# Optimization experiments

Measured on AMD Instinct MI355X. Metric: run time of the kernel, lower is better.

Reference implementation:

```python
import jax, jax.numpy as jnp
import numpy as np

HEADS = 16
CHUNK = 128  # chunked (mathematically exact) form of the causal cumsum linear attention
EPS = 0.001


def _linear_attention(q, k, v):
    # q, k, v: (B, H, L, d); q, k already SiLU-featurized
    B, H, L, d = q.shape
    Nc = L // CHUNK
    qc = q.reshape(B, H, Nc, CHUNK, d)
    kc = k.reshape(B, H, Nc, CHUNK, d)
    vc = v.reshape(B, H, Nc, CHUNK, d)

    # inter-chunk running state: S = cumsum of k (x) v over previous chunks, z = cumsum of k
    kv_chunk = jnp.einsum('bhncd,bhnce->bhnde', kc, vc)        # (B,H,Nc,d,d)
    S = jnp.cumsum(kv_chunk, axis=2) - kv_chunk                 # exclusive cumsum
    k_sum = kc.sum(axis=3)                                      # (B,H,Nc,d)
    z = jnp.cumsum(k_sum, axis=2) - k_sum                       # exclusive cumsum

    # intra-chunk causal part
    scores = jnp.einsum('bhnid,bhnjd->bhnij', qc, kc)           # (B,H,Nc,C,C)
    mask = jnp.tril(jnp.ones((CHUNK, CHUNK), dtype=bool))
    scores = jnp.where(mask, scores, jnp.zeros((), scores.dtype))
    num = jnp.einsum('bhnij,bhnje->bhnie', scores, vc)
    num = num + jnp.einsum('bhnid,bhnde->bhnie', qc, S)

    k_cum_local = jnp.cumsum(kc, axis=3)                        # within-chunk cumsum of k
    den = jnp.einsum('bhnid,bhnid->bhni', qc, k_cum_local)
    den = den + jnp.einsum('bhnid,bhnd->bhni', qc, z)

    out = num / jnp.maximum(den, EPS)[..., None]
    return out.reshape(B, H, L, d)


def setup_inputs() -> dict:
    key = jax.random.key(0)
    ks = jax.random.split(key, 9)
    D = 1024
    B, L = 4, 2048
    s = 0.02  # init scale
    return {
        'x':  jax.random.normal(ks[0], (B, L, D), dtype=jnp.float32),
        'Wq': jax.random.normal(ks[1], (D, D), dtype=jnp.float32) * s,
        'bq': jnp.zeros((D,), dtype=jnp.float32),
        'Wk': jax.random.normal(ks[2], (D, D), dtype=jnp.float32) * s,
        'bk': jnp.zeros((D,), dtype=jnp.float32),
        'Wv': jax.random.normal(ks[3], (D, D), dtype=jnp.float32) * s,
        'bv': jnp.zeros((D,), dtype=jnp.float32),
        'Wo': jax.random.normal(ks[4], (D, D), dtype=jnp.float32) * s,
        'bo': jnp.zeros((D,), dtype=jnp.float32),
    }


def reference(x, Wq, bq, Wk, bk, Wv, bv, Wo, bo):
    B, L, D = x.shape
    H = HEADS
    d = D // H
    # torch Linear: y = x @ W.T + b
    q = jax.nn.silu(x @ Wq.T + bq).reshape(B, L, H, d).transpose(0, 2, 1, 3)
    k = jax.nn.silu(x @ Wk.T + bk).reshape(B, L, H, d).transpose(0, 2, 1, 3)
    v = (x @ Wv.T + bv).reshape(B, L, H, d).transpose(0, 2, 1, 3)
    out = _linear_attention(q, k, v)                  # (B,H,L,d)
    out = out.transpose(0, 2, 1, 3).reshape(B, L, D)
    return out @ Wo.T + bo
```

## Files before the change

kernel.cpp:

```cpp
#include <hip/hip_runtime.h>
#include <math.h>

#define D_MODEL 1024
#define HEADS   16
#define HDIM    64
#define CHUNK   128
#define B_SZ    4
#define L_SEQ   2048
#define NCHUNK  16
#define NTOK    8192
#define EPS_DEN 1e-3f

typedef _Float16 half8 __attribute__((ext_vector_type(8)));
typedef float    f32x4 __attribute__((ext_vector_type(4)));

__device__ __forceinline__ void gld_lds16(const void* g, void* l) {
    __builtin_amdgcn_global_load_lds(
        (const __attribute__((address_space(1))) void*)g,
        (__attribute__((address_space(3))) void*)l, 16, 0, 0);
}

__global__ __launch_bounds__(256) void prep(
    const float* __restrict__ x,  const float* __restrict__ Wq,
    const float* __restrict__ Wk, const float* __restrict__ Wv,
    const float* __restrict__ Wo, const float* __restrict__ bq,
    const float* __restrict__ bk,
    _Float16* __restrict__ x2,  _Float16* __restrict__ w2q,
    _Float16* __restrict__ w2k, _Float16* __restrict__ wv16,
    _Float16* __restrict__ wo16, float* __restrict__ bqk) {
    const int bid = blockIdx.x;
    if (bid < 5120) {
        const float* src; _Float16* dst; int t;
        if (bid < 4096)      { src = x;  dst = x2;  t = bid * 256 + threadIdx.x; }
        else if (bid < 4608) { src = Wq; dst = w2q; t = (bid - 4096) * 256 + threadIdx.x; }
        else                 { src = Wk; dst = w2k; t = (bid - 4608) * 256 + threadIdx.x; }
        int m = t >> 7, kc = (t & 127) << 3;
        const float* s = src + (size_t)m * 1024 + kc;
        f32x4 a = *(const f32x4*)s;
        f32x4 b = *(const f32x4*)(s + 4);
        float xs[8] = {a.x, a.y, a.z, a.w, b.x, b.y, b.z, b.w};
        half8 hi, lo;
        #pragma unroll
        for (int u = 0; u < 8; ++u) {
            _Float16 h = (_Float16)xs[u];
            hi[u] = h;
            lo[u] = (_Float16)(xs[u] - (float)h);
        }
        *(half8*)(dst + (size_t)m * 2048 + kc)        = hi;
        *(half8*)(dst + (size_t)m * 2048 + 1024 + kc) = lo;
    } else if (bid < 6144) {
        const float* src; _Float16* dst; int t;
        if (bid < 5632) { src = Wv; dst = wv16; t = (bid - 5120) * 256 + threadIdx.x; }
        else            { src = Wo; dst = wo16; t = (bid - 5632) * 256 + threadIdx.x; }
        int m = t >> 7, kc = (t & 127) << 3;
        const float* s = src + (size_t)m * 1024 + kc;
        f32x4 a = *(const f32x4*)s;
        f32x4 b = *(const f32x4*)(s + 4);
        float xs[8] = {a.x, a.y, a.z, a.w, b.x, b.y, b.z, b.w};
        half8 hv;
        #pragma unroll
        for (int u = 0; u < 8; ++u) hv[u] = (_Float16)xs[u];
        *(half8*)(dst + (size_t)m * 1024 + kc) = hv;
    } else {
        int i = (bid - 6144) * 256 + threadIdx.x;
        bqk[i] = (i < 1024) ? bq[i] : bk[i - 1024];
    }
}

__global__ __launch_bounds__(256, 4) void gemm_qkv(
    const _Float16* __restrict__ A,
    const _Float16* __restrict__ Bqk,
    const _Float16* __restrict__ Bv,
    const float* __restrict__ bqk, const float* __restrict__ bv,
    float* __restrict__ Q32, float* __restrict__ K32,
    _Float16* __restrict__ Q16, _Float16* __restrict__ K16,
    _Float16* __restrict__ V16, float* __restrict__ ksum) {
    __shared__ __align__(16) _Float16 sA[4096];
    __shared__ __align__(16) _Float16 sB[4096];
    __shared__ __align__(16) _Float16 sC16[32 * 136];
    __shared__ float sksum[2][128];

    const int cb   = blockIdx.y;
    const int isqk = (cb < 16);
    const int isk  = (cb >= 8 && cb < 16);
    const int tid  = threadIdx.x;
    const int lane = tid & 63;
    const int w    = tid >> 6;
    const int row0 = blockIdx.x * 128;
    const int col0 = cb * 128;
    const int wm   = (w & 1) * 64;
    const int wn   = (w >> 1) * 64;

    const _Float16* B = isqk ? Bqk : Bv;
    const int ldb     = isqk ? 2048 : 1024;
    const int bcol0   = isqk ? col0 : col0 - 2048;
    const int kits    = isqk ? 96 : 32;

    const int ch0 = w * 64 + lane;
    const int rS0 = ch0 >> 2;
    const int cS0 = (ch0 & 3) ^ ((rS0 >> 1) & 3);
    const int ch1 = ch0 + 256;
    const int rS1 = ch1 >> 2;
    const int cS1 = (ch1 & 3) ^ ((rS1 >> 1) & 3);

    f32x4 acc[4][4];
    #pragma unroll
    for (int i = 0; i < 4; ++i)
        #pragma unroll
        for (int j = 0; j < 4; ++j) { f32x4 z = {0.f, 0.f, 0.f, 0.f}; acc[i][j] = z; }

    const int ml = lane & 15;
    const int kg = lane >> 4;
    int offA[4], offB[4];
    #pragma unroll
    for (int i = 0; i < 4; ++i) {
        int r  = wm + i * 16 + ml;
        offA[i] = r * 32 + (kg ^ ((r >> 1) & 3)) * 8;
        int rn = wn + i * 16 + ml;
        offB[i] = rn * 32 + (kg ^ ((rn >> 1) & 3)) * 8;
    }

    for (int kit = 0; kit < kits; ++kit) {
        const int k0   = kit * 32;
        const int acol = (k0 < 2048) ? k0 : k0 - 2048;
        const int bcol = (k0 < 1024) ? k0 : k0 - 1024;

        gld_lds16(A + (size_t)(row0 + rS0) * 2048 + acol + cS0 * 8, &sA[w * 512]);
        gld_lds16(A + (size_t)(row0 + rS1) * 2048 + acol + cS1 * 8, &sA[2048 + w * 512]);
        gld_lds16(B + (size_t)(bcol0 + rS0) * ldb + bcol + cS0 * 8, &sB[w * 512]);
        gld_lds16(B + (size_t)(bcol0 + rS1) * ldb + bcol + cS1 * 8, &sB[2048 + w * 512]);
        __syncthreads();

        half8 af[4], bf[4];
        #pragma unroll
        for (int i = 0; i < 4; ++i) {
            af[i] = *(const half8*)&sA[offA[i]];
            bf[i] = *(const half8*)&sB[offB[i]];
        }
        #pragma unroll
        for (int i = 0; i < 4; ++i)
            #pragma unroll
            for (int j = 0; j < 4; ++j)
                acc[i][j] = __builtin_amdgcn_mfma_f32_16x16x32_f16(af[i], bf[j], acc[i][j], 0, 0, 0);
        __syncthreads();
    }

    const int colq = isqk ? ((col0 < 1024) ? col0 : col0 - 1024) : (col0 - 2048);
    float*    Y32  = (col0 < 1024) ? Q32 : K32;
    _Float16* Y16  = isqk ? ((col0 < 1024) ? Q16 : K16) : V16;

    const int rg = lane >> 4;
    #pragma unroll
    for (int j = 0; j < 4; ++j) {
        const float bvb = isqk ? bqk[col0 + wn + j * 16 + ml]
                               : bv[colq + wn + j * 16 + ml];
        const int nn = colq + wn + j * 16 + ml;
        #pragma unroll
        for (int i = 0; i < 4; ++i) {
            #pragma unroll
            for (int t = 0; t < 4; ++t) {
                float vv = acc[i][j][t] + bvb;
                if (isqk) {
                    vv = vv / (1.f + expf(-vv));
                    int mm = row0 + wm + i * 16 + rg * 4 + t;
                    Y32[(size_t)mm * 1024 + nn] = vv;
                }
                acc[i][j][t] = vv;
            }
        }
    }

    if (isk) {
        #pragma unroll
        for (int j = 0; j < 4; ++j) {
            float ps = 0.f;
            #pragma unroll
            for (int i = 0; i < 4; ++i)
                #pragma unroll
                for (int t = 0; t < 4; ++t) ps += acc[i][j][t];
            ps += __shfl_xor(ps, 16, 64);
            ps += __shfl_xor(ps, 32, 64);
            if (kg == 0) sksum[wm >> 6][wn + j * 16 + ml] = ps;
        }
        __syncthreads();
        if (tid < 128) {
            const int b = row0 >> 11;
            const int n = (row0 >> 7) & 15;
            const int cg = colq + tid;
            const int h = cg >> 6, f = cg & 63;
            ksum[(size_t)(((b * 16 + h) * 16 + n)) * 64 + f] =
                sksum[0][tid] + sksum[1][tid];
        }
        __syncthreads();
    }

    for (int s = 0; s < 4; ++s) {
        if ((wm == 0) == (s < 2)) {
            const int ib = (s & 1) * 2;
            #pragma unroll
            for (int ii = 0; ii < 2; ++ii)
                #pragma unroll
                for (int j = 0; j < 4; ++j)
                    #pragma unroll
                    for (int t = 0; t < 4; ++t) {
                        int lr = ii * 16 + rg * 4 + t;
                        sC16[lr * 136 + wn + j * 16 + ml] = (_Float16)acc[ib + ii][j][t];
                    }
        }
        __syncthreads();
        #pragma unroll
        for (int u = 0; u < 2; ++u) {
            int c = u * 256 + tid;
            int r = c >> 4, cc = (c & 15) * 8;
            half8 hv = *(const half8*)&sC16[r * 136 + cc];
            *(half8*)(Y16 + (size_t)(row0 + 32 * s + r) * 1024 + colq + cc) = hv;
        }
        __syncthreads();
    }
}

__global__ __launch_bounds__(256, 4) void gemm_out(
    const _Float16* __restrict__ A,
    const _Float16* __restrict__ B,
    const float* __restrict__ bias,
    float* __restrict__ Y) {
    __shared__ __align__(16) _Float16 sA[4096];
    __shared__ __align__(16) _Float16 sB[2048];

    const int tid  = threadIdx.x;
    const int lane = tid & 63;
    const int w    = tid >> 6;
    const int row0 = blockIdx.x * 128;
    const int col0 = blockIdx.y * 64;

    const int ch0 = w * 64 + lane;
    const int rS0 = ch0 >> 2;
    const int cS0 = (ch0 & 3) ^ ((rS0 >> 1) & 3);
    const int ch1 = ch0 + 256;
    const int rS1 = ch1 >> 2;
    const int cS1 = (ch1 & 3) ^ ((rS1 >> 1) & 3);

    f32x4 acc[2][4];
    #pragma unroll
    for (int i = 0; i < 2; ++i)
        #pragma unroll
        for (int j = 0; j < 4; ++j) { f32x4 z = {0.f, 0.f, 0.f, 0.f}; acc[i][j] = z; }

    const int ml = lane & 15;
    const int kg = lane >> 4;
    int offA[2], offB[4];
    #pragma unroll
    for (int i = 0; i < 2; ++i) {
        int r  = w * 32 + i * 16 + ml;
        offA[i] = r * 32 + (kg ^ ((r >> 1) & 3)) * 8;
    }
    #pragma unroll
    for (int j = 0; j < 4; ++j) {
        int rn = j * 16 + ml;
        offB[j] = rn * 32 + (kg ^ ((rn >> 1) & 3)) * 8;
    }

    for (int kit = 0; kit < 32; ++kit) {
        const int k0 = kit * 32;
        gld_lds16(A + (size_t)(row0 + rS0) * 1024 + k0 + cS0 * 8, &sA[w * 512]);
        gld_lds16(A + (size_t)(row0 + rS1) * 1024 + k0 + cS1 * 8, &sA[2048 + w * 512]);
        gld_lds16(B + (size_t)(col0 + rS0) * 1024 + k0 + cS0 * 8, &sB[w * 512]);
        __syncthreads();

        half8 af[2], bf[4];
        #pragma unroll
        for (int i = 0; i < 2; ++i) af[i] = *(const half8*)&sA[offA[i]];
        #pragma unroll
        for (int j = 0; j < 4; ++j) bf[j] = *(const half8*)&sB[offB[j]];
        #pragma unroll
        for (int i = 0; i < 2; ++i)
            #pragma unroll
            for (int j = 0; j < 4; ++j)
                acc[i][j] = __builtin_amdgcn_mfma_f32_16x16x32_f16(af[i], bf[j], acc[i][j], 0, 0, 0);
        __syncthreads();
    }

    const int rg = lane >> 4;
    #pragma unroll
    for (int j = 0; j < 4; ++j) {
        const int nn = col0 + j * 16 + ml;
        const float bvb = bias[nn];
        #pragma unroll
        for (int i = 0; i < 2; ++i) {
            #pragma unroll
            for (int t = 0; t < 4; ++t) {
                int mm = row0 + w * 32 + i * 16 + rg * 4 + t;
                Y[(size_t)mm * 1024 + nn] = acc[i][j][t] * 64.f + bvb;
            }
        }
    }
}

__global__ __launch_bounds__(256) void chunk_stats(
    const _Float16* __restrict__ k16g, const _Float16* __restrict__ v16g,
    float* __restrict__ kvT) {
    const int blk = blockIdx.x;
    const int n = blk & 15, bh = blk >> 4, h = bh & 15, b = bh >> 4;
    const size_t base = ((size_t)b * L_SEQ + (size_t)n * CHUNK) * D_MODEL + (size_t)h * HDIM;

    __shared__ __align__(16) _Float16 sv[64 * 136];
    __shared__ __align__(16) _Float16 sk[64 * 136];

    const int tid = threadIdx.x;
    #pragma unroll
    for (int p = 0; p < 4; ++p) {
        int idx = p * 256 + tid;
        int j = idx >> 3, c = idx & 7;
        half8 vv = *(const half8*)(v16g + base + (size_t)j * D_MODEL + c * 8);
        half8 kk = *(const half8*)(k16g + base + (size_t)j * D_MODEL + c * 8);
        #pragma unroll
        for (int u = 0; u < 8; ++u) {
            sv[(c * 8 + u) * 136 + j] = vv[u];
            sk[(c * 8 + u) * 136 + j] = kk[u];
        }
    }
    __syncthreads();

    const int lane = tid & 63;
    const int w    = tid >> 6;
    const int ml   = lane & 15;
    const int kg   = lane >> 4;

    f32x4 acc[4];
    #pragma unroll
    for (int ft = 0; ft < 4; ++ft) { f32x4 z = {0.f,0.f,0.f,0.f}; acc[ft] = z; }
    #pragma unroll
    for (int ft = 0; ft < 4; ++ft)
        #pragma unroll
        for (int kit = 0; kit < 4; ++kit) {
            half8 af = *(const half8*)&sv[(w * 16 + ml) * 136 + kit * 32 + kg * 8];
            half8 bf = *(const half8*)&sk[(ft * 16 + ml) * 136 + kit * 32 + kg * 8];
            acc[ft] = __builtin_amdgcn_mfma_f32_16x16x32_f16(af, bf, acc[ft], 0, 0, 0);
        }
    float* o = kvT + (size_t)blk * 4096;
    #pragma unroll
    for (int ft = 0; ft < 4; ++ft)
        #pragma unroll
        for (int t = 0; t < 4; ++t) {
            int e = w * 16 + kg * 4 + t;
            o[e * 64 + ft * 16 + ml] = acc[ft][t];
        }
}

__global__ __launch_bounds__(256) void scan_chunks(float* __restrict__ kvT,
                                                   float* __restrict__ ksum) {
    const int bh  = blockIdx.x >> 4;
    const int seg = blockIdx.x & 15;
    const int idx = seg * 256 + threadIdx.x;
    float* base = kvT + (size_t)bh * NCHUNK * 4096 + idx;
    float run = 0.f;
    #pragma unroll
    for (int nn = 0; nn < NCHUNK; ++nn) {
        float t = base[(size_t)nn * 4096];
        base[(size_t)nn * 4096] = run;
        run += t;
    }
    if (seg == 0 && threadIdx.x < 64) {
        float* zb = ksum + (size_t)bh * NCHUNK * 64 + threadIdx.x;
        float r2 = 0.f;
        #pragma unroll
        for (int nn = 0; nn < NCHUNK; ++nn) {
            float t = zb[nn * 64];
            zb[nn * 64] = r2;
            r2 += t;
        }
    }
}

__global__ __launch_bounds__(256) void den_kernel(
    const float* __restrict__ qf32, const float* __restrict__ kf32,
    const float* __restrict__ zg, float* __restrict__ deng) {
    const int blk = blockIdx.x;
    const int n = blk & 15, bh = blk >> 4, h = bh & 15, b = bh >> 4;
    const size_t base = ((size_t)b * L_SEQ + (size_t)n * CHUNK) * D_MODEL + (size_t)h * HDIM;

    __shared__ float skk[128 * 64];
    __shared__ float part[4 * 64];

    const int tid = threadIdx.x;
    #pragma unroll
    for (int p = 0; p < 8; ++p) {
        int idx = p * 256 + tid;
        int j = idx >> 4, fc = (idx & 15) * 4;
        *(f32x4*)&skk[j * 64 + fc] = *(const f32x4*)(kf32 + base + (size_t)j * D_MODEL + fc);
    }
    __syncthreads();

    const int w = tid >> 6, lane = tid & 63;
    float ps = 0.f;
    for (int j = w * 32; j < w * 32 + 32; ++j) ps += skk[j * 64 + lane];
    part[w * 64 + lane] = ps;
    __syncthreads();

    float acc = zg[(size_t)blk * 64 + lane];
    for (int w2 = 0; w2 < w; ++w2) acc += part[w2 * 64 + lane];

    float* dout = deng + ((size_t)(b * 16 + h)) * L_SEQ + n * CHUNK;
    for (int jj = 0; jj < 32; ++jj) {
        int j = w * 32 + jj;
        acc += skk[j * 64 + lane];
        float d = qf32[base + (size_t)j * D_MODEL + lane] * acc;
        #pragma unroll
        for (int off = 32; off > 0; off >>= 1) d += __shfl_xor(d, off, 64);
        if (lane == 0) dout[j] = d;
    }
}

__global__ __launch_bounds__(256) void attn_core(
    const _Float16* __restrict__ q16g, const _Float16* __restrict__ k16g,
    const _Float16* __restrict__ v16g, const float* __restrict__ STg,
    const float* __restrict__ deng, _Float16* __restrict__ O16) {
    const int blk = blockIdx.x;
    const int n = blk & 15, bh = blk >> 4, h = bh & 15, b = bh >> 4;
    const size_t base = ((size_t)b * L_SEQ + (size_t)n * CHUNK) * D_MODEL + (size_t)h * HDIM;

    __shared__ __align__(16) _Float16 sq [128 * 72];
    __shared__ __align__(16) _Float16 sk [128 * 72];
    __shared__ __align__(16) _Float16 sv [64 * 136];
    __shared__ __align__(16) _Float16 sS [64 * 72];
    __shared__ __align__(16) _Float16 ssc[64 * 136];
    __shared__ float sden[128];

    const int tid = threadIdx.x;
    #pragma unroll
    for (int p = 0; p < 4; ++p) {
        int idx = p * 256 + tid;
        int j = idx >> 3, c = idx & 7;
        *(half8*)&sq[j * 72 + c * 8] = *(const half8*)(q16g + base + (size_t)j * D_MODEL + c * 8);
        *(half8*)&sk[j * 72 + c * 8] = *(const half8*)(k16g + base + (size_t)j * D_MODEL + c * 8);
        half8 vv = *(const half8*)(v16g + base + (size_t)j * D_MODEL + c * 8);
        #pragma unroll
        for (int u = 0; u < 8; ++u) sv[(c * 8 + u) * 136 + j] = vv[u];
    }
    #pragma unroll
    for (int p = 0; p < 2; ++p) {
        int idx = p * 256 + tid;
        int e = idx >> 3, c = idx & 7;
        f32x4 a = *(const f32x4*)(STg + (size_t)blk * 4096 + e * 64 + c * 8);
        f32x4 b4 = *(const f32x4*)(STg + (size_t)blk * 4096 + e * 64 + c * 8 + 4);
        half8 hv;
        hv[0] = (_Float16)a.x;  hv[1] = (_Float16)a.y;
        hv[2] = (_Float16)a.z;  hv[3] = (_Float16)a.w;
        hv[4] = (_Float16)b4.x; hv[5] = (_Float16)b4.y;
        hv[6] = (_Float16)b4.z; hv[7] = (_Float16)b4.w;
        *(half8*)&sS[e * 72 + c * 8] = hv;
    }
    if (tid < 128) sden[tid] = deng[((size_t)(b * 16 + h)) * L_SEQ + n * CHUNK + tid];
    __syncthreads();

    const int lane = tid & 63;
    const int w    = tid >> 6;
    const int ml   = lane & 15;
    const int kg   = lane >> 4;

    for (int h2 = 0; h2 < 2; ++h2) {
        const int r0 = h2 * 64 + w * 16;
        const int rowmax = r0 + 15;

        f32x4 acc1[8];
        #pragma unroll
        for (int nt = 0; nt < 8; ++nt) { f32x4 z = {0.f,0.f,0.f,0.f}; acc1[nt] = z; }
        #pragma unroll
        for (int nt = 0; nt < 8; ++nt) {
            if (nt * 16 <= rowmax) {
                #pragma unroll
                for (int kit = 0; kit < 2; ++kit) {
                    half8 af = *(const half8*)&sq[(r0 + ml) * 72 + kit * 32 + kg * 8];
                    half8 bf = *(const half8*)&sk[(nt * 16 + ml) * 72 + kit * 32 + kg * 8];
                    acc1[nt] = __builtin_amdgcn_mfma_f32_16x16x32_f16(af, bf, acc1[nt], 0, 0, 0);
                }
            }
        }
        #pragma unroll
        for (int nt = 0; nt < 8; ++nt) {
            #pragma unroll
            for (int t = 0; t < 4; ++t) {
                int lr = w * 16 + kg * 4 + t;
                int ig = h2 * 64 + lr;
                int jg = nt * 16 + ml;
                float val = (jg <= ig) ? acc1[nt][t] : 0.f;
                ssc[lr * 136 + jg] = (_Float16)val;
            }
        }
        __syncthreads();

        f32x4 acc2[4];
        #pragma unroll
        for (int et = 0; et < 4; ++et) { f32x4 z = {0.f,0.f,0.f,0.f}; acc2[et] = z; }
        const int nkit = (h2 == 0) ? 2 : 4;
        #pragma unroll
        for (int et = 0; et < 4; ++et) {
            for (int kit = 0; kit < nkit; ++kit) {
                half8 af = *(const half8*)&ssc[(w * 16 + ml) * 136 + kit * 32 + kg * 8];
                half8 bf = *(const half8*)&sv[(et * 16 + ml) * 136 + kit * 32 + kg * 8];
                acc2[et] = __builtin_amdgcn_mfma_f32_16x16x32_f16(af, bf, acc2[et], 0, 0, 0);
            }
            #pragma unroll
            for (int kit = 0; kit < 2; ++kit) {
                half8 af = *(const half8*)&sq[(r0 + ml) * 72 + kit * 32 + kg * 8];
                half8 bf = *(const half8*)&sS[(et * 16 + ml) * 72 + kit * 32 + kg * 8];
                acc2[et] = __builtin_amdgcn_mfma_f32_16x16x32_f16(af, bf, acc2[et], 0, 0, 0);
            }
        }
        #pragma unroll
        for (int t = 0; t < 4; ++t) {
            int lr = w * 16 + kg * 4 + t;
            int ig = h2 * 64 + lr;
            float rc = 0.015625f / fmaxf(sden[ig], EPS_DEN);
            #pragma unroll
            for (int et = 0; et < 4; ++et) {
                int e = et * 16 + ml;
                O16[base + (size_t)ig * D_MODEL + e] = (_Float16)(acc2[et][t] * rc);
            }
        }
        __syncthreads();
    }
}

extern "C" void kernel_launch(void* const* d_in, const int* in_sizes, int n_in,
                              void* d_out, int out_size, void* d_ws, size_t ws_size,
                              hipStream_t stream) {
    const float* x  = (const float*)d_in[0];
    const float* Wq = (const float*)d_in[1];
    const float* bq = (const float*)d_in[2];
    const float* Wk = (const float*)d_in[3];
    const float* bk = (const float*)d_in[4];
    const float* Wv = (const float*)d_in[5];
    const float* bv = (const float*)d_in[6];
    const float* Wo = (const float*)d_in[7];
    const float* bo = (const float*)d_in[8];
    float* out = (float*)d_out;

    char* p = (char*)d_ws;
    _Float16* x2   = (_Float16*)p;  p += (size_t)NTOK * 2048 * 2;
    _Float16* w2q  = (_Float16*)p;  p += (size_t)1024 * 2048 * 2;
    _Float16* w2k  = (_Float16*)p;  p += (size_t)1024 * 2048 * 2;
    _Float16* wv16 = (_Float16*)p;  p += (size_t)1024 * 1024 * 2;
    _Float16* wo16 = (_Float16*)p;  p += (size_t)1024 * 1024 * 2;
    float* qf   = (float*)p;        p += (size_t)NTOK * 1024 * 4;
    float* kf   = (float*)p;        p += (size_t)NTOK * 1024 * 4;
    _Float16* q16 = (_Float16*)p;   p += (size_t)NTOK * 1024 * 2;
    _Float16* k16 = (_Float16*)p;   p += (size_t)NTOK * 1024 * 2;
    _Float16* v16 = (_Float16*)p;   p += (size_t)NTOK * 1024 * 2;
    float* kvT  = (float*)p;        p += (size_t)1024 * 4096 * 4;
    float* ksb  = (float*)p;        p += (size_t)1024 * 64 * 4;
    float* den  = (float*)p;        p += (size_t)B_SZ * HEADS * L_SEQ * 4;
    float* bqk  = (float*)p;        p += 2048 * 4;
    _Float16* attn16 = x2;

    prep<<<6152, 256, 0, stream>>>(x, Wq, Wk, Wv, Wo, bq, bk,
                                   x2, w2q, w2k, wv16, wo16, bqk);

    gemm_qkv<<<dim3(64, 24), 256, 0, stream>>>(x2, w2q, wv16, bqk, bv,
                                               qf, kf, q16, k16, v16, ksb);

    chunk_stats<<<1024, 256, 0, stream>>>(k16, v16, kvT);
    scan_chunks<<<1024, 256, 0, stream>>>(kvT, ksb);
    den_kernel<<<1024, 256, 0, stream>>>(qf, kf, ksb, den);
    attn_core<<<1024, 256, 0, stream>>>(q16, k16, v16, kvT, den, attn16);

    gemm_out<<<dim3(64, 16), 256, 0, stream>>>(attn16, wo16, bo, out);
}
```

Before: 348.1 us.

## Rework QKV GEMM into 256x256 tiles with 4-stage async LDS pipeline

Changes the QKV projection GEMM from 128x128 tiles with 256 threads to 256x256 tiles with 512 threads. A 4-buffer global_load_lds pipeline keeps three stages in flight, paced by vmcnt waits and a single barrier per k-step. A 1D swizzled block index groups blocks for L2 reuse. The k-sum reduction now writes directly without an LDS round trip. The aim is to cut per-iteration barrier stalls and raise operand reuse, at the cost of 128 KB of LDS and more accumulator registers per thread, which limits occupancy.

```diff
diff --git a/kernel.cpp b/kernel.cpp
--- a/kernel.cpp
+++ b/kernel.cpp
@@ -67,7 +67,7 @@
     }
 }
 
-__global__ __launch_bounds__(256, 4) void gemm_qkv(
+__global__ __launch_bounds__(512, 2) void gemm_qkv(
     const _Float16* __restrict__ A,
     const _Float16* __restrict__ Bqk,
     const _Float16* __restrict__ Bv,
@@ -75,94 +75,106 @@
     float* __restrict__ Q32, float* __restrict__ K32,
     _Float16* __restrict__ Q16, _Float16* __restrict__ K16,
     _Float16* __restrict__ V16, float* __restrict__ ksum) {
-    __shared__ __align__(16) _Float16 sA[4096];
-    __shared__ __align__(16) _Float16 sB[4096];
-    __shared__ __align__(16) _Float16 sC16[32 * 136];
-    __shared__ float sksum[2][128];
-
-    const int cb   = blockIdx.y;
-    const int isqk = (cb < 16);
-    const int isk  = (cb >= 8 && cb < 16);
+    __shared__ __align__(16) _Float16 sbuf[4 * 16384];
+
+    const int bid = blockIdx.x;
+    const int swz = (bid & 7) * 48 + (bid >> 3);
+    const int isqk = (swz < 256);
+    const int lin  = isqk ? swz : (swz - 256);
+    const int bx   = lin & 31;
+    const int cb   = lin >> 5;
+    const int row0 = bx * 256;
+    const int col0 = isqk ? cb * 256 : 2048 + cb * 256;
+
     const int tid  = threadIdx.x;
     const int lane = tid & 63;
     const int w    = tid >> 6;
-    const int row0 = blockIdx.x * 128;
-    const int col0 = cb * 128;
-    const int wm   = (w & 1) * 64;
+    const int wm   = (w & 1) * 128;
     const int wn   = (w >> 1) * 64;
 
-    const _Float16* B = isqk ? Bqk : Bv;
-    const int ldb     = isqk ? 2048 : 1024;
-    const int bcol0   = isqk ? col0 : col0 - 2048;
-    const int kits    = isqk ? 96 : 32;
-
-    const int ch0 = w * 64 + lane;
-    const int rS0 = ch0 >> 2;
-    const int cS0 = (ch0 & 3) ^ ((rS0 >> 1) & 3);
-    const int ch1 = ch0 + 256;
-    const int rS1 = ch1 >> 2;
-    const int cS1 = (ch1 & 3) ^ ((rS1 >> 1) & 3);
-
-    f32x4 acc[4][4];
-    #pragma unroll
-    for (int i = 0; i < 4; ++i)
-        #pragma unroll
-        for (int j = 0; j < 4; ++j) { f32x4 z = {0.f, 0.f, 0.f, 0.f}; acc[i][j] = z; }
+    const _Float16* Bm = isqk ? Bqk : Bv;
+    const int ldb      = isqk ? 2048 : 1024;
+    const int brow0    = isqk ? col0 : col0 - 2048;
+    const int NT       = isqk ? 96 : 32;
+
+    const int rS = tid >> 2;
+    const int cS = (tid & 3) ^ ((rS >> 1) & 3);
+    const _Float16* gA = A  + (size_t)(row0  + rS) * 2048 + cS * 8;
+    const _Float16* gB = Bm + (size_t)(brow0 + rS) * ldb  + cS * 8;
+    const size_t stepA = (size_t)128 * 2048;
+    const size_t stepB = (size_t)128 * ldb;
+
+    auto stage = [&](int t) {
+        const int k0   = t * 32;
+        const int acol = (isqk && k0 >= 2048) ? k0 - 2048 : k0;
+        const int bcol = (isqk && k0 >= 1024) ? k0 - 1024 : k0;
+        _Float16* l = sbuf + (t & 3) * 16384;
+        gld_lds16(gA + acol,         l + w * 512);
+        gld_lds16(gA + stepA + acol, l + 4096  + w * 512);
+        gld_lds16(gB + bcol,         l + 8192  + w * 512);
+        gld_lds16(gB + stepB + bcol, l + 12288 + w * 512);
+    };
 
     const int ml = lane & 15;
     const int kg = lane >> 4;
-    int offA[4], offB[4];
-    #pragma unroll
-    for (int i = 0; i < 4; ++i) {
-        int r  = wm + i * 16 + ml;
+    int offA[8], offB[4];
+    #pragma unroll
+    for (int i = 0; i < 8; ++i) {
+        int r = wm + i * 16 + ml;
         offA[i] = r * 32 + (kg ^ ((r >> 1) & 3)) * 8;
-        int rn = wn + i * 16 + ml;
-        offB[i] = rn * 32 + (kg ^ ((rn >> 1) & 3)) * 8;
-    }
-
-    for (int kit = 0; kit < kits; ++kit) {
-        const int k0   = kit * 32;
-        const int acol = (k0 < 2048) ? k0 : k0 - 2048;
-        const int bcol = (k0 < 1024) ? k0 : k0 - 1024;
-
-        gld_lds16(A + (size_t)(row0 + rS0) * 2048 + acol + cS0 * 8, &sA[w * 512]);
-        gld_lds16(A + (size_t)(row0 + rS1) * 2048 + acol + cS1 * 8, &sA[2048 + w * 512]);
-        gld_lds16(B + (size_t)(bcol0 + rS0) * ldb + bcol + cS0 * 8, &sB[w * 512]);
-        gld_lds16(B + (size_t)(bcol0 + rS1) * ldb + bcol + cS1 * 8, &sB[2048 + w * 512]);
-        __syncthreads();
-
-        half8 af[4], bf[4];
-        #pragma unroll
-        for (int i = 0; i < 4; ++i) {
-            af[i] = *(const half8*)&sA[offA[i]];
-            bf[i] = *(const half8*)&sB[offB[i]];
-        }
-        #pragma unroll
-        for (int i = 0; i < 4; ++i)
+    }
+    #pragma unroll
+    for (int j = 0; j < 4; ++j) {
+        int rn = wn + j * 16 + ml;
+        offB[j] = 8192 + rn * 32 + (kg ^ ((rn >> 1) & 3)) * 8;
+    }
+
+    f32x4 acc[8][4];
+    #pragma unroll
+    for (int i = 0; i < 8; ++i)
+        #pragma unroll
+        for (int j = 0; j < 4; ++j) { f32x4 z = {0.f, 0.f, 0.f, 0.f}; acc[i][j] = z; }
+
+    stage(0); stage(1); stage(2);
+
+    #pragma unroll 4
+    for (int t = 0; t < NT; ++t) {
+        asm volatile("s_waitcnt vmcnt(8)\n\ts_barrier" ::: "memory");
+        if (t + 3 < NT) stage(t + 3);
+        const _Float16* lb = sbuf + (t & 3) * 16384;
+        half8 af[8], bf[4];
+        #pragma unroll
+        for (int i = 0; i < 8; ++i) af[i] = *(const half8*)&lb[offA[i]];
+        #pragma unroll
+        for (int j = 0; j < 4; ++j) bf[j] = *(const half8*)&lb[offB[j]];
+        __builtin_amdgcn_s_setprio(1);
+        #pragma unroll
+        for (int i = 0; i < 8; ++i)
             #pragma unroll
             for (int j = 0; j < 4; ++j)
                 acc[i][j] = __builtin_amdgcn_mfma_f32_16x16x32_f16(af[i], bf[j], acc[i][j], 0, 0, 0);
-        __syncthreads();
-    }
+        __builtin_amdgcn_s_setprio(0);
+    }
+    asm volatile("s_waitcnt vmcnt(0)" ::: "memory");
+    __syncthreads();
 
     const int colq = isqk ? ((col0 < 1024) ? col0 : col0 - 1024) : (col0 - 2048);
     float*    Y32  = (col0 < 1024) ? Q32 : K32;
     _Float16* Y16  = isqk ? ((col0 < 1024) ? Q16 : K16) : V16;
 
-    const int rg = lane >> 4;
     #pragma unroll
     for (int j = 0; j < 4; ++j) {
         const float bvb = isqk ? bqk[col0 + wn + j * 16 + ml]
                                : bv[colq + wn + j * 16 + ml];
         const int nn = colq + wn + j * 16 + ml;
         #pragma unroll
-        for (int i = 0; i < 4; ++i) {
+        for (int i = 0; i < 8; ++i) {
             #pragma unroll
             for (int t = 0; t < 4; ++t) {
                 float vv = acc[i][j][t] + bvb;
                 if (isqk) {
                     vv = vv / (1.f + expf(-vv));
-                    int mm = row0 + wm + i * 16 + rg * 4 + t;
+                    int mm = row0 + wm + i * 16 + kg * 4 + t;
                     Y32[(size_t)mm * 1024 + nn] = vv;
                 }
                 acc[i][j][t] = vv;
@@ -170,50 +182,46 @@
         }
     }
 
-    if (isk) {
+    if (isqk && col0 >= 1024) {
+        const int rowg = row0 + wm;
+        const int b = rowg >> 11, n = (rowg >> 7) & 15;
         #pragma unroll
         for (int j = 0; j < 4; ++j) {
             float ps = 0.f;
             #pragma unroll
-            for (int i = 0; i < 4; ++i)
+            for (int i = 0; i < 8; ++i)
                 #pragma unroll
                 for (int t = 0; t < 4; ++t) ps += acc[i][j][t];
             ps += __shfl_xor(ps, 16, 64);
             ps += __shfl_xor(ps, 32, 64);
-            if (kg == 0) sksum[wm >> 6][wn + j * 16 + ml] = ps;
-        }
-        __syncthreads();
-        if (tid < 128) {
-            const int b = row0 >> 11;
-            const int n = (row0 >> 7) & 15;
-            const int cg = colq + tid;
-            const int h = cg >> 6, f = cg & 63;
-            ksum[(size_t)(((b * 16 + h) * 16 + n)) * 64 + f] =
-                sksum[0][tid] + sksum[1][tid];
-        }
-        __syncthreads();
-    }
-
-    for (int s = 0; s < 4; ++s) {
-        if ((wm == 0) == (s < 2)) {
-            const int ib = (s & 1) * 2;
+            if (kg == 0) {
+                const int cg = colq + wn + j * 16 + ml;
+                const int h = cg >> 6, f = cg & 63;
+                ksum[(size_t)((b * 16 + h) * 16 + n) * 64 + f] = ps;
+            }
+        }
+    }
+
+    _Float16* sl = sbuf;
+    for (int s = 0; s < 8; ++s) {
+        if ((w & 1) == (s >> 2)) {
+            const int i0 = (s & 3) * 2;
             #pragma unroll
             for (int ii = 0; ii < 2; ++ii)
                 #pragma unroll
                 for (int j = 0; j < 4; ++j)
                     #pragma unroll
-                    for (int t = 0; t < 4; ++t) {
-                        int lr = ii * 16 + rg * 4 + t;
-                        sC16[lr * 136 + wn + j * 16 + ml] = (_Float16)acc[ib + ii][j][t];
-                    }
+                    for (int t = 0; t < 4; ++t)
+                        sl[(ii * 16 + kg * 4 + t) * 264 + wn + j * 16 + ml] =
+                            (_Float16)acc[i0 + ii][j][t];
         }
         __syncthreads();
-        #pragma unroll
-        for (int u = 0; u < 2; ++u) {
-            int c = u * 256 + tid;
-            int r = c >> 4, cc = (c & 15) * 8;
-            half8 hv = *(const half8*)&sC16[r * 136 + cc];
-            *(half8*)(Y16 + (size_t)(row0 + 32 * s + r) * 1024 + colq + cc) = hv;
+        {
+            const int r = tid >> 4, c0 = (tid & 15) * 16;
+            half8 h0 = *(const half8*)&sl[r * 264 + c0];
+            half8 h1 = *(const half8*)&sl[r * 264 + c0 + 8];
+            *(half8*)(Y16 + (size_t)(row0 + s * 32 + r) * 1024 + colq + c0)     = h0;
+            *(half8*)(Y16 + (size_t)(row0 + s * 32 + r) * 1024 + colq + c0 + 8) = h1;
         }
         __syncthreads();
     }
@@ -556,8 +564,8 @@
     prep<<<6152, 256, 0, stream>>>(x, Wq, Wk, Wv, Wo, bq, bk,
                                    x2, w2q, w2k, wv16, wo16, bqk);
 
-    gemm_qkv<<<dim3(64, 24), 256, 0, stream>>>(x2, w2q, wv16, bqk, bv,
-                                               qf, kf, q16, k16, v16, ksb);
+    gemm_qkv<<<384, 512, 0, stream>>>(x2, w2q, wv16, bqk, bv,
+                                      qf, kf, q16, k16, v16, ksb);
 
     chunk_stats<<<1024, 256, 0, stream>>>(k16, v16, kvT);
     scan_chunks<<<1024, 256, 0, stream>>>(kvT, ksb);
```

After: 396.5 us. 1.14x slower.

## Triple-buffer LDS loads in QKV and output GEMMs with a single barrier per step

Applied to the files above, without the earlier changes.

Both GEMM kernels now prefetch global-to-LDS tiles two K-steps ahead into a three-slot ring buffer. Each step does one explicit waitcnt plus barrier instead of two __syncthreads, so load latency overlaps with MFMA work. MFMA sections are wrapped in s_setprio to favour math issue. The cost is more LDS per block, and the QKV kernel's occupancy hint drops from 4 to 3 blocks. Correctness depends on the hand-written vmcnt values matching the number of outstanding loads.

```diff
diff --git a/kernel.cpp b/kernel.cpp
--- a/kernel.cpp
+++ b/kernel.cpp
@@ -67,7 +67,7 @@
     }
 }
 
-__global__ __launch_bounds__(256, 4) void gemm_qkv(
+__global__ __launch_bounds__(256, 3) void gemm_qkv(
     const _Float16* __restrict__ A,
     const _Float16* __restrict__ Bqk,
     const _Float16* __restrict__ Bv,
@@ -75,10 +75,9 @@
     float* __restrict__ Q32, float* __restrict__ K32,
     _Float16* __restrict__ Q16, _Float16* __restrict__ K16,
     _Float16* __restrict__ V16, float* __restrict__ ksum) {
-    __shared__ __align__(16) _Float16 sA[4096];
-    __shared__ __align__(16) _Float16 sB[4096];
-    __shared__ __align__(16) _Float16 sC16[32 * 136];
+    __shared__ __align__(16) _Float16 sbuf[3 * 8192];
     __shared__ float sksum[2][128];
+    _Float16* sC16 = sbuf;
 
     const int cb   = blockIdx.y;
     const int isqk = (cb < 16);
@@ -91,10 +90,10 @@
     const int wm   = (w & 1) * 64;
     const int wn   = (w >> 1) * 64;
 
-    const _Float16* B = isqk ? Bqk : Bv;
-    const int ldb     = isqk ? 2048 : 1024;
-    const int bcol0   = isqk ? col0 : col0 - 2048;
-    const int kits    = isqk ? 96 : 32;
+    const _Float16* Bm = isqk ? Bqk : Bv;
+    const int ldb      = isqk ? 2048 : 1024;
+    const int bcol0    = isqk ? col0 : col0 - 2048;
+    const int kits     = isqk ? 96 : 32;
 
     const int ch0 = w * 64 + lane;
     const int rS0 = ch0 >> 2;
@@ -103,11 +102,21 @@
     const int rS1 = ch1 >> 2;
     const int cS1 = (ch1 & 3) ^ ((rS1 >> 1) & 3);
 
-    f32x4 acc[4][4];
-    #pragma unroll
-    for (int i = 0; i < 4; ++i)
-        #pragma unroll
-        for (int j = 0; j < 4; ++j) { f32x4 z = {0.f, 0.f, 0.f, 0.f}; acc[i][j] = z; }
+    const _Float16* gA0 = A  + (size_t)(row0  + rS0) * 2048 + cS0 * 8;
+    const _Float16* gA1 = A  + (size_t)(row0  + rS1) * 2048 + cS1 * 8;
+    const _Float16* gB0 = Bm + (size_t)(bcol0 + rS0) * ldb  + cS0 * 8;
+    const _Float16* gB1 = Bm + (size_t)(bcol0 + rS1) * ldb  + cS1 * 8;
+
+    auto stage = [&](int kt) {
+        const int k0   = kt * 32;
+        const int acol = (k0 < 2048) ? k0 : k0 - 2048;
+        const int bcol = (k0 < 1024) ? k0 : k0 - 1024;
+        _Float16* l = sbuf + (kt % 3) * 8192;
+        gld_lds16(gA0 + acol, l + w * 512);
+        gld_lds16(gA1 + acol, l + 2048 + w * 512);
+        gld_lds16(gB0 + bcol, l + 4096 + w * 512);
+        gld_lds16(gB1 + bcol, l + 6144 + w * 512);
+    };
 
     const int ml = lane & 15;
     const int kg = lane >> 4;
@@ -117,33 +126,41 @@
         int r  = wm + i * 16 + ml;
         offA[i] = r * 32 + (kg ^ ((r >> 1) & 3)) * 8;
         int rn = wn + i * 16 + ml;
-        offB[i] = rn * 32 + (kg ^ ((rn >> 1) & 3)) * 8;
-    }
-
-    for (int kit = 0; kit < kits; ++kit) {
-        const int k0   = kit * 32;
-        const int acol = (k0 < 2048) ? k0 : k0 - 2048;
-        const int bcol = (k0 < 1024) ? k0 : k0 - 1024;
-
-        gld_lds16(A + (size_t)(row0 + rS0) * 2048 + acol + cS0 * 8, &sA[w * 512]);
-        gld_lds16(A + (size_t)(row0 + rS1) * 2048 + acol + cS1 * 8, &sA[2048 + w * 512]);
-        gld_lds16(B + (size_t)(bcol0 + rS0) * ldb + bcol + cS0 * 8, &sB[w * 512]);
-        gld_lds16(B + (size_t)(bcol0 + rS1) * ldb + bcol + cS1 * 8, &sB[2048 + w * 512]);
-        __syncthreads();
-
+        offB[i] = 4096 + rn * 32 + (kg ^ ((rn >> 1) & 3)) * 8;
+    }
+
+    f32x4 acc[4][4];
+    #pragma unroll
+    for (int i = 0; i < 4; ++i)
+        #pragma unroll
+        for (int j = 0; j < 4; ++j) { f32x4 z = {0.f, 0.f, 0.f, 0.f}; acc[i][j] = z; }
+
+    auto compute = [&](int kt) {
+        const _Float16* lb = sbuf + (kt % 3) * 8192;
         half8 af[4], bf[4];
         #pragma unroll
         for (int i = 0; i < 4; ++i) {
-            af[i] = *(const half8*)&sA[offA[i]];
-            bf[i] = *(const half8*)&sB[offB[i]];
-        }
+            af[i] = *(const half8*)&lb[offA[i]];
+            bf[i] = *(const half8*)&lb[offB[i]];
+        }
+        __builtin_amdgcn_s_setprio(1);
         #pragma unroll
         for (int i = 0; i < 4; ++i)
             #pragma unroll
             for (int j = 0; j < 4; ++j)
                 acc[i][j] = __builtin_amdgcn_mfma_f32_16x16x32_f16(af[i], bf[j], acc[i][j], 0, 0, 0);
-        __syncthreads();
-    }
+        __builtin_amdgcn_s_setprio(0);
+    };
+
+    stage(0); stage(1);
+    for (int t = 0; t < kits - 1; ++t) {
+        asm volatile("s_waitcnt vmcnt(4) lgkmcnt(0)\n\ts_barrier" ::: "memory");
+        if (t + 2 < kits) stage(t + 2);
+        compute(t);
+    }
+    asm volatile("s_waitcnt vmcnt(0) lgkmcnt(0)\n\ts_barrier" ::: "memory");
+    compute(kits - 1);
+    __syncthreads();
 
     const int colq = isqk ? ((col0 < 1024) ? col0 : col0 - 1024) : (col0 - 2048);
     float*    Y32  = (col0 < 1024) ? Q32 : K32;
@@ -224,8 +241,7 @@
     const _Float16* __restrict__ B,
     const float* __restrict__ bias,
     float* __restrict__ Y) {
-    __shared__ __align__(16) _Float16 sA[4096];
-    __shared__ __align__(16) _Float16 sB[2048];
+    __shared__ __align__(16) _Float16 sbuf[3 * 6144];
 
     const int tid  = threadIdx.x;
     const int lane = tid & 63;
@@ -240,6 +256,18 @@
     const int rS1 = ch1 >> 2;
     const int cS1 = (ch1 & 3) ^ ((rS1 >> 1) & 3);
 
+    const _Float16* gA0 = A + (size_t)(row0 + rS0) * 1024 + cS0 * 8;
+    const _Float16* gA1 = A + (size_t)(row0 + rS1) * 1024 + cS1 * 8;
+    const _Float16* gB0 = B + (size_t)(col0 + rS0) * 1024 + cS0 * 8;
+
+    auto stage = [&](int kt) {
+        const int k0 = kt * 32;
+        _Float16* l = sbuf + (kt % 3) * 6144;
+        gld_lds16(gA0 + k0, l + w * 512);
+        gld_lds16(gA1 + k0, l + 2048 + w * 512);
+        gld_lds16(gB0 + k0, l + 4096 + w * 512);
+    };
+
     f32x4 acc[2][4];
     #pragma unroll
     for (int i = 0; i < 2; ++i)
@@ -257,28 +285,33 @@
     #pragma unroll
     for (int j = 0; j < 4; ++j) {
         int rn = j * 16 + ml;
-        offB[j] = rn * 32 + (kg ^ ((rn >> 1) & 3)) * 8;
-    }
-
-    for (int kit = 0; kit < 32; ++kit) {
-        const int k0 = kit * 32;
-        gld_lds16(A + (size_t)(row0 + rS0) * 1024 + k0 + cS0 * 8, &sA[w * 512]);
-        gld_lds16(A + (size_t)(row0 + rS1) * 1024 + k0 + cS1 * 8, &sA[2048 + w * 512]);
-        gld_lds16(B + (size_t)(col0 + rS0) * 1024 + k0 + cS0 * 8, &sB[w * 512]);
-        __syncthreads();
-
+        offB[j] = 4096 + rn * 32 + (kg ^ ((rn >> 1) & 3)) * 8;
+    }
+
+    auto compute = [&](int kt) {
+        const _Float16* lb = sbuf + (kt % 3) * 6144;
         half8 af[2], bf[4];
         #pragma unroll
-        for (int i = 0; i < 2; ++i) af[i] = *(const half8*)&sA[offA[i]];
-        #pragma unroll
-        for (int j = 0; j < 4; ++j) bf[j] = *(const half8*)&sB[offB[j]];
+        for (int i = 0; i < 2; ++i) af[i] = *(const half8*)&lb[offA[i]];
+        #pragma unroll
+        for (int j = 0; j < 4; ++j) bf[j] = *(const half8*)&lb[offB[j]];
+        __builtin_amdgcn_s_setprio(1);
         #pragma unroll
         for (int i = 0; i < 2; ++i)
             #pragma unroll
             for (int j = 0; j < 4; ++j)
                 acc[i][j] = __builtin_amdgcn_mfma_f32_16x16x32_f16(af[i], bf[j], acc[i][j], 0, 0, 0);
-        __syncthreads();
-    }
+        __builtin_amdgcn_s_setprio(0);
+    };
+
+    stage(0); stage(1);
+    for (int t = 0; t < 31; ++t) {
+        asm volatile("s_waitcnt vmcnt(3) lgkmcnt(0)\n\ts_barrier" ::: "memory");
+        if (t + 2 < 32) stage(t + 2);
+        compute(t);
+    }
+    asm volatile("s_waitcnt vmcnt(0) lgkmcnt(0)\n\ts_barrier" ::: "memory");
+    compute(31);
 
     const int rg = lane >> 4;
     #pragma unroll
```

After: 364.4 us. 4.7% more time.

## Fuse denominator into attention core with split-fp16 hi/lo corrections; widen output GEMM tile

Applied to the files above, without the earlier changes.

Drops the fp32 Q/K buffers and the separate denominator kernel. gemm_qkv now stores the fp16 residual (lo part) of SiLU(q) and SiLU(k) next to the fp16 values, and attn_core gets the causal denominator from extra hi*lo MFMA cross terms plus a row reduction against the chunk prefix z. This removes a kernel launch and the 64 MB of fp32 Q/K traffic, at the cost of extra MFMAs and uncached global reads of the lo parts inside attn_core. It also enlarges the gemm_out tile to 128x128 with 4x4 MFMA per wave, which halves the grid and raises reuse.

```diff
diff --git a/kernel.cpp b/kernel.cpp
--- a/kernel.cpp
+++ b/kernel.cpp
@@ -12,6 +12,7 @@
 #define EPS_DEN 1e-3f
 
 typedef _Float16 half8 __attribute__((ext_vector_type(8)));
+typedef _Float16 half4 __attribute__((ext_vector_type(4)));
 typedef float    f32x4 __attribute__((ext_vector_type(4)));
 
 __device__ __forceinline__ void gld_lds16(const void* g, void* l) {
@@ -72,7 +73,7 @@
     const _Float16* __restrict__ Bqk,
     const _Float16* __restrict__ Bv,
     const float* __restrict__ bqk, const float* __restrict__ bv,
-    float* __restrict__ Q32, float* __restrict__ K32,
+    _Float16* __restrict__ Qlo, _Float16* __restrict__ Klo,
     _Float16* __restrict__ Q16, _Float16* __restrict__ K16,
     _Float16* __restrict__ V16, float* __restrict__ ksum) {
     __shared__ __align__(16) _Float16 sA[4096];
@@ -146,7 +147,7 @@
     }
 
     const int colq = isqk ? ((col0 < 1024) ? col0 : col0 - 1024) : (col0 - 2048);
-    float*    Y32  = (col0 < 1024) ? Q32 : K32;
+    _Float16* Ylo  = (col0 < 1024) ? Qlo : Klo;
     _Float16* Y16  = isqk ? ((col0 < 1024) ? Q16 : K16) : V16;
 
     const int rg = lane >> 4;
@@ -163,7 +164,8 @@
                 if (isqk) {
                     vv = vv / (1.f + expf(-vv));
                     int mm = row0 + wm + i * 16 + rg * 4 + t;
-                    Y32[(size_t)mm * 1024 + nn] = vv;
+                    _Float16 hv = (_Float16)vv;
+                    Ylo[(size_t)mm * 1024 + nn] = (_Float16)(vv - (float)hv);
                 }
                 acc[i][j][t] = vv;
             }
@@ -225,13 +227,15 @@
     const float* __restrict__ bias,
     float* __restrict__ Y) {
     __shared__ __align__(16) _Float16 sA[4096];
-    __shared__ __align__(16) _Float16 sB[2048];
+    __shared__ __align__(16) _Float16 sB[4096];
 
     const int tid  = threadIdx.x;
     const int lane = tid & 63;
     const int w    = tid >> 6;
     const int row0 = blockIdx.x * 128;
-    const int col0 = blockIdx.y * 64;
+    const int col0 = blockIdx.y * 128;
+    const int wm   = (w & 1) * 64;
+    const int wn   = (w >> 1) * 64;
 
     const int ch0 = w * 64 + lane;
     const int rS0 = ch0 >> 2;
@@ -240,24 +244,21 @@
     const int rS1 = ch1 >> 2;
     const int cS1 = (ch1 & 3) ^ ((rS1 >> 1) & 3);
 
-    f32x4 acc[2][4];
-    #pragma unroll
-    for (int i = 0; i < 2; ++i)
+    f32x4 acc[4][4];
+    #pragma unroll
+    for (int i = 0; i < 4; ++i)
         #pragma unroll
         for (int j = 0; j < 4; ++j) { f32x4 z = {0.f, 0.f, 0.f, 0.f}; acc[i][j] = z; }
 
     const int ml = lane & 15;
     const int kg = lane >> 4;
-    int offA[2], offB[4];
-    #pragma unroll
-    for (int i = 0; i < 2; ++i) {
-        int r  = w * 32 + i * 16 + ml;
+    int offA[4], offB[4];
+    #pragma unroll
+    for (int i = 0; i < 4; ++i) {
+        int r  = wm + i * 16 + ml;
         offA[i] = r * 32 + (kg ^ ((r >> 1) & 3)) * 8;
-    }
-    #pragma unroll
-    for (int j = 0; j < 4; ++j) {
-        int rn = j * 16 + ml;
-        offB[j] = rn * 32 + (kg ^ ((rn >> 1) & 3)) * 8;
+        int rn = wn + i * 16 + ml;
+        offB[i] = rn * 32 + (kg ^ ((rn >> 1) & 3)) * 8;
     }
 
     for (int kit = 0; kit < 32; ++kit) {
@@ -265,15 +266,17 @@
         gld_lds16(A + (size_t)(row0 + rS0) * 1024 + k0 + cS0 * 8, &sA[w * 512]);
         gld_lds16(A + (size_t)(row0 + rS1) * 1024 + k0 + cS1 * 8, &sA[2048 + w * 512]);
         gld_lds16(B + (size_t)(col0 + rS0) * 1024 + k0 + cS0 * 8, &sB[w * 512]);
-        __syncthreads();
-
-        half8 af[2], bf[4];
-        #pragma unroll
-        for (int i = 0; i < 2; ++i) af[i] = *(const half8*)&sA[offA[i]];
-        #pragma unroll
-        for (int j = 0; j < 4; ++j) bf[j] = *(const half8*)&sB[offB[j]];
-        #pragma unroll
-        for (int i = 0; i < 2; ++i)
+        gld_lds16(B + (size_t)(col0 + rS1) * 1024 + k0 + cS1 * 8, &sB[2048 + w * 512]);
+        __syncthreads();
+
+        half8 af[4], bf[4];
+        #pragma unroll
+        for (int i = 0; i < 4; ++i) {
+            af[i] = *(const half8*)&sA[offA[i]];
+            bf[i] = *(const half8*)&sB[offB[i]];
+        }
+        #pragma unroll
+        for (int i = 0; i < 4; ++i)
             #pragma unroll
             for (int j = 0; j < 4; ++j)
                 acc[i][j] = __builtin_amdgcn_mfma_f32_16x16x32_f16(af[i], bf[j], acc[i][j], 0, 0, 0);
@@ -283,13 +286,13 @@
     const int rg = lane >> 4;
     #pragma unroll
     for (int j = 0; j < 4; ++j) {
-        const int nn = col0 + j * 16 + ml;
+        const int nn = col0 + wn + j * 16 + ml;
         const float bvb = bias[nn];
         #pragma unroll
-        for (int i = 0; i < 2; ++i) {
+        for (int i = 0; i < 4; ++i) {
             #pragma unroll
             for (int t = 0; t < 4; ++t) {
-                int mm = row0 + w * 32 + i * 16 + rg * 4 + t;
+                int mm = row0 + wm + i * 16 + rg * 4 + t;
                 Y[(size_t)mm * 1024 + nn] = acc[i][j][t] * 64.f + bvb;
             }
         }
@@ -372,49 +375,11 @@
     }
 }
 
-__global__ __launch_bounds__(256) void den_kernel(
-    const float* __restrict__ qf32, const float* __restrict__ kf32,
-    const float* __restrict__ zg, float* __restrict__ deng) {
-    const int blk = blockIdx.x;
-    const int n = blk & 15, bh = blk >> 4, h = bh & 15, b = bh >> 4;
-    const size_t base = ((size_t)b * L_SEQ + (size_t)n * CHUNK) * D_MODEL + (size_t)h * HDIM;
-
-    __shared__ float skk[128 * 64];
-    __shared__ float part[4 * 64];
-
-    const int tid = threadIdx.x;
-    #pragma unroll
-    for (int p = 0; p < 8; ++p) {
-        int idx = p * 256 + tid;
-        int j = idx >> 4, fc = (idx & 15) * 4;
-        *(f32x4*)&skk[j * 64 + fc] = *(const f32x4*)(kf32 + base + (size_t)j * D_MODEL + fc);
-    }
-    __syncthreads();
-
-    const int w = tid >> 6, lane = tid & 63;
-    float ps = 0.f;
-    for (int j = w * 32; j < w * 32 + 32; ++j) ps += skk[j * 64 + lane];
-    part[w * 64 + lane] = ps;
-    __syncthreads();
-
-    float acc = zg[(size_t)blk * 64 + lane];
-    for (int w2 = 0; w2 < w; ++w2) acc += part[w2 * 64 + lane];
-
-    float* dout = deng + ((size_t)(b * 16 + h)) * L_SEQ + n * CHUNK;
-    for (int jj = 0; jj < 32; ++jj) {
-        int j = w * 32 + jj;
-        acc += skk[j * 64 + lane];
-        float d = qf32[base + (size_t)j * D_MODEL + lane] * acc;
-        #pragma unroll
-        for (int off = 32; off > 0; off >>= 1) d += __shfl_xor(d, off, 64);
-        if (lane == 0) dout[j] = d;
-    }
-}
-
 __global__ __launch_bounds__(256) void attn_core(
     const _Float16* __restrict__ q16g, const _Float16* __restrict__ k16g,
-    const _Float16* __restrict__ v16g, const float* __restrict__ STg,
-    const float* __restrict__ deng, _Float16* __restrict__ O16) {
+    const _Float16* __restrict__ v16g, const _Float16* __restrict__ qlog,
+    const _Float16* __restrict__ klog, const float* __restrict__ STg,
+    const float* __restrict__ zg, _Float16* __restrict__ O16) {
     const int blk = blockIdx.x;
     const int n = blk & 15, bh = blk >> 4, h = bh & 15, b = bh >> 4;
     const size_t base = ((size_t)b * L_SEQ + (size_t)n * CHUNK) * D_MODEL + (size_t)h * HDIM;
@@ -424,7 +389,7 @@
     __shared__ __align__(16) _Float16 sv [64 * 136];
     __shared__ __align__(16) _Float16 sS [64 * 72];
     __shared__ __align__(16) _Float16 ssc[64 * 136];
-    __shared__ float sden[128];
+    __shared__ float szz[64];
 
     const int tid = threadIdx.x;
     #pragma unroll
@@ -450,7 +415,7 @@
         hv[6] = (_Float16)b4.z; hv[7] = (_Float16)b4.w;
         *(half8*)&sS[e * 72 + c * 8] = hv;
     }
-    if (tid < 128) sden[tid] = deng[((size_t)(b * 16 + h)) * L_SEQ + n * CHUNK + tid];
+    if (tid < 64) szz[tid] = zg[(size_t)blk * 64 + tid];
     __syncthreads();
 
     const int lane = tid & 63;
@@ -461,6 +426,10 @@
     for (int h2 = 0; h2 < 2; ++h2) {
         const int r0 = h2 * 64 + w * 16;
         const int rowmax = r0 + 15;
+
+        half8 aflo[2];
+        aflo[0] = *(const half8*)(qlog + base + (size_t)(r0 + ml) * D_MODEL + kg * 8);
+        aflo[1] = *(const half8*)(qlog + base + (size_t)(r0 + ml) * D_MODEL + 32 + kg * 8);
 
         f32x4 acc1[8];
         #pragma unroll
@@ -478,6 +447,45 @@
         }
         #pragma unroll
         for (int nt = 0; nt < 8; ++nt) {
+            if (nt * 16 <= rowmax) {
+                const _Float16* kb = klog + base + (size_t)(nt * 16 + ml) * D_MODEL;
+                half8 bl0 = *(const half8*)(kb + kg * 8);
+                half8 bl1 = *(const half8*)(kb + 32 + kg * 8);
+                half8 ah0 = *(const half8*)&sq[(r0 + ml) * 72 + kg * 8];
+                half8 ah1 = *(const half8*)&sq[(r0 + ml) * 72 + 32 + kg * 8];
+                half8 bh0 = *(const half8*)&sk[(nt * 16 + ml) * 72 + kg * 8];
+                half8 bh1 = *(const half8*)&sk[(nt * 16 + ml) * 72 + 32 + kg * 8];
+                acc1[nt] = __builtin_amdgcn_mfma_f32_16x16x32_f16(ah0, bl0, acc1[nt], 0, 0, 0);
+                acc1[nt] = __builtin_amdgcn_mfma_f32_16x16x32_f16(ah1, bl1, acc1[nt], 0, 0, 0);
+                acc1[nt] = __builtin_amdgcn_mfma_f32_16x16x32_f16(aflo[0], bh0, acc1[nt], 0, 0, 0);
+                acc1[nt] = __builtin_amdgcn_mfma_f32_16x16x32_f16(aflo[1], bh1, acc1[nt], 0, 0, 0);
+            }
+        }
+
+        float rs[4];
+        #pragma unroll
+        for (int t = 0; t < 4; ++t) {
+            const int ig = r0 + kg * 4 + t;
+            float s = 0.f;
+            #pragma unroll
+            for (int nt = 0; nt < 8; ++nt) {
+                int jg = nt * 16 + ml;
+                s += (jg <= ig) ? acc1[nt][t] : 0.f;
+            }
+            const int f0 = ml * 4;
+            half4 ql = *(const half4*)(qlog + base + (size_t)ig * D_MODEL + f0);
+            #pragma unroll
+            for (int u = 0; u < 4; ++u)
+                s += ((float)sq[ig * 72 + f0 + u] + (float)ql[u]) * szz[f0 + u];
+            s += __shfl_xor(s, 1, 64);
+            s += __shfl_xor(s, 2, 64);
+            s += __shfl_xor(s, 4, 64);
+            s += __shfl_xor(s, 8, 64);
+            rs[t] = s;
+        }
+
+        #pragma unroll
+        for (int nt = 0; nt < 8; ++nt) {
             #pragma unroll
             for (int t = 0; t < 4; ++t) {
                 int lr = w * 16 + kg * 4 + t;
@@ -511,7 +519,7 @@
         for (int t = 0; t < 4; ++t) {
             int lr = w * 16 + kg * 4 + t;
             int ig = h2 * 64 + lr;
-            float rc = 0.015625f / fmaxf(sden[ig], EPS_DEN);
+            float rc = 0.015625f / fmaxf(rs[t], EPS_DEN);
             #pragma unroll
             for (int et = 0; et < 4; ++et) {
                 int e = et * 16 + ml;
@@ -542,14 +550,13 @@
     _Float16* w2k  = (_Float16*)p;  p += (size_t)1024 * 2048 * 2;
     _Float16* wv16 = (_Float16*)p;  p += (size_t)1024 * 1024 * 2;
     _Float16* wo16 = (_Float16*)p;  p += (size_t)1024 * 1024 * 2;
-    float* qf   = (float*)p;        p += (size_t)NTOK * 1024 * 4;
-    float* kf   = (float*)p;        p += (size_t)NTOK * 1024 * 4;
-    _Float16* q16 = (_Float16*)p;   p += (size_t)NTOK * 1024 * 2;
-    _Float16* k16 = (_Float16*)p;   p += (size_t)NTOK * 1024 * 2;
-    _Float16* v16 = (_Float16*)p;   p += (size_t)NTOK * 1024 * 2;
+    _Float16* qlo  = (_Float16*)p;  p += (size_t)NTOK * 1024 * 2;
+    _Float16* klo  = (_Float16*)p;  p += (size_t)NTOK * 1024 * 2;
+    _Float16* q16  = (_Float16*)p;  p += (size_t)NTOK * 1024 * 2;
+    _Float16* k16  = (_Float16*)p;  p += (size_t)NTOK * 1024 * 2;
+    _Float16* v16  = (_Float16*)p;  p += (size_t)NTOK * 1024 * 2;
     float* kvT  = (float*)p;        p += (size_t)1024 * 4096 * 4;
     float* ksb  = (float*)p;        p += (size_t)1024 * 64 * 4;
-    float* den  = (float*)p;        p += (size_t)B_SZ * HEADS * L_SEQ * 4;
     float* bqk  = (float*)p;        p += 2048 * 4;
     _Float16* attn16 = x2;
 
@@ -557,12 +564,11 @@
                                    x2, w2q, w2k, wv16, wo16, bqk);
 
     gemm_qkv<<<dim3(64, 24), 256, 0, stream>>>(x2, w2q, wv16, bqk, bv,
-                                               qf, kf, q16, k16, v16, ksb);
+                                               qlo, klo, q16, k16, v16, ksb);
 
     chunk_stats<<<1024, 256, 0, stream>>>(k16, v16, kvT);
     scan_chunks<<<1024, 256, 0, stream>>>(kvT, ksb);
-    den_kernel<<<1024, 256, 0, stream>>>(qf, kf, ksb, den);
-    attn_core<<<1024, 256, 0, stream>>>(q16, k16, v16, kvT, den, attn16);
-
-    gemm_out<<<dim3(64, 16), 256, 0, stream>>>(attn16, wo16, bo, out);
-}
+    attn_core<<<1024, 256, 0, stream>>>(q16, k16, v16, qlo, klo, kvT, ksb, attn16);
+
+    gemm_out<<<dim3(64, 8), 256, 0, stream>>>(attn16, wo16, bo, out);
+}
```

Result: no change. 346.6 us (-0.4%).
